# Kernel tuning notes

Measured on AMD Instinct MI355X. Metric: run time of the kernel, lower is better.

Reference implementation:

```python
import jax, jax.numpy as jnp
import numpy as np

HEAD_DIM = 128
NUM_Q_HEAD = 32
NUM_KV_HEAD = 8
GROUP_SIZE = 128
EPS = 1e-5
WINDOW = 512
CAP = 50.0
CLIP_L, CLIP_R = -0.01, 1.01
SCALE = 1.0 / np.sqrt(HEAD_DIM)
NEG = -1e9


def group_rmsnorm(x, gamma, gsz, eps):
    # x: [B, S, H]; per-group RMS over contiguous chunks of size gsz, then learned scale
    b, s, h = x.shape
    xg = x.reshape(b, s, h // gsz, gsz)
    rms = jnp.sqrt(jnp.mean(xg * xg, axis=-1, keepdims=True) + eps)
    return (xg / rms).reshape(b, s, h) * gamma


def setup_inputs() -> dict:
    key = jax.random.key(0)
    k1, k2, k3, k4, k5 = jax.random.split(key, 5)
    B, S = 2, 2048
    q = jax.random.normal(k1, (B, S, NUM_Q_HEAD, HEAD_DIM), dtype=jnp.float32)
    k = jax.random.normal(k2, (B, S, NUM_KV_HEAD, HEAD_DIM), dtype=jnp.float32)
    v = jax.random.normal(k3, (B, S, NUM_KV_HEAD, HEAD_DIM), dtype=jnp.float32)
    # GroupRMSNorm weights ~ U(init_range) = U(-1, 1)
    gamma_q = jax.random.uniform(k4, (NUM_Q_HEAD * HEAD_DIM,), dtype=jnp.float32, minval=-1.0, maxval=1.0)
    gamma_k = jax.random.uniform(k5, (NUM_KV_HEAD * HEAD_DIM,), dtype=jnp.float32, minval=-1.0, maxval=1.0)
    return {"q": q, "k": k, "v": v, "gamma_q": gamma_q, "gamma_k": gamma_k}


def reference(q, k, v, gamma_q, gamma_k):
    B, Sq, Hq, D = q.shape
    Sk, Hkv = k.shape[1], k.shape[2]
    # QK GroupRMSNorm on flattened hidden dim
    qn = group_rmsnorm(q.reshape(B, Sq, Hq * D), gamma_q, GROUP_SIZE, EPS).reshape(B, Sq, Hq, D)
    kn = group_rmsnorm(k.reshape(B, Sk, Hkv * D), gamma_k, GROUP_SIZE, EPS).reshape(B, Sk, Hkv, D)
    # GQA: repeat_interleave kv heads to match q heads
    rep = Hq // Hkv
    kr = jnp.repeat(kn, rep, axis=2)
    vr = jnp.repeat(v, rep, axis=2)
    # scores: [B, H, Sq, Sk]
    logits = jnp.einsum('bqhd,bkhd->bhqk', qn, kr) * SCALE
    # softmax capping (temperature path skipped when cap is set)
    logits = jnp.tanh(logits / CAP) * CAP
    # causal + sliding-window mask (aligned at sequence end)
    i = jnp.arange(Sq)[:, None]
    j = jnp.arange(Sk)[None, :]
    pos = i + (Sk - Sq)
    allowed = (j <= pos) & (pos - j <= WINDOW)
    logits = jnp.where(allowed, logits, NEG)
    probs = jax.nn.softmax(logits.astype(jnp.float32), axis=-1)
    # softmax clipping: clamp(probs * (r - l) + l, 0, 1)
    probs = jnp.clip(probs * (CLIP_R - CLIP_L) + CLIP_L, 0.0, 1.0)
    # output: [B, Sq, H, D]
    o = jnp.einsum('bhqk,bkhd->bqhd', probs.astype(q.dtype), vr)
    return o
```

## Files before the change

kernel.cpp:

```cpp
#include <hip/hip_runtime.h>

#define SEQ     2048
#define NQH     32
#define NKV     8
#define HD      128
#define WINDOW  512
#define QT      64
#define EPS_F   1e-5f
#define CQ2     0.12752981793f
#define PSTR    72

#define KN_OFF  0ull
#define VT_OFF  8388608ull

#define ROWPAT(r, hg) ((((r) & 3) + 8 * ((r) >> 2)) + 4 * (hg))

#define WAIT_BAR_4() asm volatile("s_waitcnt vmcnt(4)\n\ts_barrier" ::: "memory")
#define WAIT_BAR_0() asm volatile("s_waitcnt vmcnt(0)\n\ts_barrier" ::: "memory")
#define LGKM_BAR()  asm volatile("s_waitcnt lgkmcnt(0)\n\ts_barrier" ::: "memory")

using bf16x4 = __attribute__((ext_vector_type(4))) __bf16;
using bf16x8 = __attribute__((ext_vector_type(8))) __bf16;
using f32x16 = __attribute__((ext_vector_type(16))) float;

__device__ __forceinline__ void dma16(const void* g, void* l) {
    __builtin_amdgcn_global_load_lds(
        (const __attribute__((address_space(1))) unsigned int*)g,
        (__attribute__((address_space(3))) unsigned int*)l, 16, 0, 0);
}

__global__ __launch_bounds__(256)
void prep(const float* __restrict__ k, const float* __restrict__ v,
          const float* __restrict__ gk,
          __bf16* __restrict__ kn, __bf16* __restrict__ vt)
{
    const int blk = blockIdx.x;
    const int tid = threadIdx.x;
    if (blk < 512) {
        const int l16  = tid & 15;
        const int rsub = tid >> 4;
        #pragma unroll
        for (int it = 0; it < 4; it++) {
            const int row = blk * 64 + it * 16 + rsub;
            const float* src = k + (size_t)row * HD + l16 * 8;
            const float* g   = gk + (row & 7) * HD + l16 * 8;
            float4 a  = *(const float4*)(src);
            float4 b4 = *(const float4*)(src + 4);
            float ss = a.x*a.x + a.y*a.y + a.z*a.z + a.w*a.w
                     + b4.x*b4.x + b4.y*b4.y + b4.z*b4.z + b4.w*b4.w;
            ss += __shfl_xor(ss, 1); ss += __shfl_xor(ss, 2);
            ss += __shfl_xor(ss, 4); ss += __shfl_xor(ss, 8);
            const float rs = rsqrtf(ss * (1.f / 128.f) + EPS_F);
            float4 g0 = *(const float4*)(g);
            float4 g1 = *(const float4*)(g + 4);
            bf16x8 o;
            o[0] = (__bf16)(a.x  * rs * g0.x);  o[1] = (__bf16)(a.y  * rs * g0.y);
            o[2] = (__bf16)(a.z  * rs * g0.z);  o[3] = (__bf16)(a.w  * rs * g0.w);
            o[4] = (__bf16)(b4.x * rs * g1.x);  o[5] = (__bf16)(b4.y * rs * g1.y);
            o[6] = (__bf16)(b4.z * rs * g1.z);  o[7] = (__bf16)(b4.w * rs * g1.w);
            *(bf16x8*)(kn + (size_t)row * HD + l16 * 8) = o;
        }
    } else {
        const int blk2 = blk - 512;
        const int b    = blk2 >> 9;
        const int kvh  = (blk2 >> 6) & 7;
        const int sc   = (blk2 >> 2) & 15;
        const int dc   = blk2 & 3;
        const int s0   = sc * 128;
        const int d0   = dc * 32;
        const int c    = tid & 7;
        const int r    = tid >> 3;

        float xs[4][4];
        const float* src = v + ((size_t)(b * SEQ + s0 + r * 4) * NKV + kvh) * HD
                           + d0 + c * 4;
        #pragma unroll
        for (int i = 0; i < 4; i++) {
            float4 x = *(const float4*)(src + (size_t)i * (NKV * HD));
            xs[i][0] = x.x; xs[i][1] = x.y; xs[i][2] = x.z; xs[i][3] = x.w;
        }
        __bf16* dstb = vt + ((size_t)((b * NKV + kvh) * HD + d0 + c * 4)) * SEQ
                       + s0 + r * 4;
        #pragma unroll
        for (int u = 0; u < 4; u++) {
            bf16x4 o;
            o[0] = (__bf16)xs[0][u]; o[1] = (__bf16)xs[1][u];
            o[2] = (__bf16)xs[2][u]; o[3] = (__bf16)xs[3][u];
            *(bf16x4*)(dstb + (size_t)u * SEQ) = o;
        }
    }
}

__global__ __launch_bounds__(256, 2)
void swa_main(const float* __restrict__ q, const __bf16* __restrict__ kn,
              const __bf16* __restrict__ vt, const float* __restrict__ gq,
              float* __restrict__ out)
{
    __shared__ __align__(16) __bf16 sKV[3][QT * HD];
    __shared__ __align__(16) __bf16 sP[QT * PSTR];
    __shared__ float sLp[2][QT];
    __shared__ float sInvL[QT];

    const int wg   = blockIdx.x;
    const int qt   = wg & 31;
    const int h    = (wg >> 5) & 31;
    const int b    = wg >> 10;
    const int kvh  = h >> 2;
    const int i0   = qt * QT;
    const int tid  = threadIdx.x;
    const int lane = tid & 63;
    const int wave = tid >> 6;
    const int mhalf = wave & 1;
    const int nhalf = wave >> 1;
    const int m    = lane & 31;
    const int hg   = lane >> 5;

    const char* k_src[4];  const char* v_src[4];
    int kq_off[4];  int v_off[4];
    {
        const char* kn_head = (const char*)kn + ((size_t)b * SEQ * NKV + kvh) * 256;
        const char* vt_head = (const char*)vt + ((size_t)(b * NKV + kvh) * HD) * (SEQ * 2);
        #pragma unroll
        for (int i = 0; i < 4; i++) {
            const int chunk = wave * 4 + i;
            {
                const int r    = chunk * 4 + (lane >> 4);
                const int cpos = lane & 15;
                const int c    = (cpos & 8) | ((cpos ^ r) & 7);
                k_src[i]  = kn_head + (size_t)r * (NKV * HD * 2) + c * 16;
                kq_off[i] = chunk * 1024;
            }
            {
                const int r    = chunk * 8 + (lane >> 3);
                const int cpos = lane & 7;
                const int c    = cpos ^ (r & 7);
                v_src[i] = vt_head + (size_t)r * (SEQ * 2) + c * 16;
                v_off[i] = chunk * 1024;
            }
        }
    }

    const int t_lo   = (i0 >= WINDOW ? (i0 - WINDOW) : 0) >> 6;
    const int t_hi   = i0 >> 6;
    const int ttbias = t_hi - 8;
    const int krow   = nhalf * 32 + m;
    const size_t kstride = (size_t)64 * (NKV * HD * 2);

    {
        const size_t ko = (size_t)t_lo * kstride;
        char* dst0 = (char*)&sKV[t_lo % 3][0];
        #pragma unroll
        for (int i = 0; i < 4; i++) dma16(k_src[i] + ko, dst0 + kq_off[i]);
        if (t_lo < t_hi) {
            char* dst1 = (char*)&sKV[(t_lo + 1) % 3][0];
            #pragma unroll
            for (int i = 0; i < 4; i++) dma16(k_src[i] + ko + kstride, dst1 + kq_off[i]);
        }
    }

    bf16x8 qf[8];
    {
        const int qrow = i0 + mhalf * 32 + m;
        const float* qp = q + ((size_t)(b * SEQ + qrow) * NQH + h) * HD;
        float4 qb[16];
        float ss = 0.0f;
        #pragma unroll
        for (int kf = 0; kf < 8; kf++) {
            const int d0 = kf * 16 + hg * 8;
            float4 a  = *(const float4*)(qp + d0);
            float4 b4 = *(const float4*)(qp + d0 + 4);
            qb[kf * 2] = a; qb[kf * 2 + 1] = b4;
            ss += a.x*a.x + a.y*a.y + a.z*a.z + a.w*a.w
                + b4.x*b4.x + b4.y*b4.y + b4.z*b4.z + b4.w*b4.w;
        }
        ss += __shfl_xor(ss, 32);
        const float rs = rsqrtf(ss * (1.f / 128.f) + EPS_F) * CQ2;
        const float* gp = gq + h * HD;
        #pragma unroll
        for (int kf = 0; kf < 8; kf++) {
            const int d0 = kf * 16 + hg * 8;
            float4 g0 = *(const float4*)(gp + d0);
            float4 g1 = *(const float4*)(gp + d0 + 4);
            bf16x8 f;
            f[0] = (__bf16)(qb[kf*2].x   * rs * g0.x);
            f[1] = (__bf16)(qb[kf*2].y   * rs * g0.y);
            f[2] = (__bf16)(qb[kf*2].z   * rs * g0.z);
            f[3] = (__bf16)(qb[kf*2].w   * rs * g0.w);
            f[4] = (__bf16)(qb[kf*2+1].x * rs * g1.x);
            f[5] = (__bf16)(qb[kf*2+1].y * rs * g1.y);
            f[6] = (__bf16)(qb[kf*2+1].z * rs * g1.z);
            f[7] = (__bf16)(qb[kf*2+1].w * rs * g1.w);
            qf[kf] = f;
        }
    }

    float lacc[16];
    #pragma unroll
    for (int i = 0; i < 16; i++) lacc[i] = 0.f;
    bf16x8 ec[9][2];

    #pragma unroll
    for (int tt = 0; tt < 9; tt++) {
        const int t = ttbias + tt;
        if (t >= t_lo) {
            if (t < t_hi) { WAIT_BAR_4(); } else { WAIT_BAR_0(); }
            const __bf16* kb = &sKV[t % 3][0];
            bf16x8 bk[8];
            #pragma unroll
            for (int kf = 0; kf < 8; kf++) {
                const int cc  = kf * 2 + hg;
                const int pos = (cc & 8) | ((cc ^ krow) & 7);
                bk[kf] = *(const bf16x8*)(kb + krow * HD + pos * 8);
            }
            if (t + 2 <= t_hi) {
                const size_t ko = (size_t)(t + 2) * kstride;
                char* dstp = (char*)&sKV[(t + 2) % 3][0];
                #pragma unroll
                for (int i = 0; i < 4; i++) dma16(k_src[i] + ko, dstp + kq_off[i]);
            }
            f32x16 c;
            #pragma unroll
            for (int i = 0; i < 16; i++) c[i] = 0.f;
            #pragma unroll
            for (int kf = 0; kf < 8; kf++)
                c = __builtin_amdgcn_mfma_f32_32x32x16_bf16(qf[kf], bk[kf], c, 0, 0, 0);

            const bool do_mask = (t == t_hi) || (t == t_lo && i0 >= WINDOW);
            const int kj = t * 64 + krow;
            float e[16];
            #pragma unroll
            for (int r = 0; r < 16; r++) {
                float ev = __builtin_amdgcn_exp2f(c[r]);
                if (do_mask) {
                    const int qi = i0 + mhalf * 32 + ROWPAT(r, hg);
                    ev = ((unsigned)(qi - kj) <= WINDOW) ? ev : 0.f;
                }
                lacc[r] += ev;
                e[r] = ev;
            }
            bf16x8 p0v, p1v;
            #pragma unroll
            for (int j = 0; j < 8; j++) { p0v[j] = (__bf16)e[j]; p1v[j] = (__bf16)e[8 + j]; }
            ec[tt][0] = p0v;  ec[tt][1] = p1v;
        }
    }

    #pragma unroll
    for (int r = 0; r < 16; r++) {
        float l = lacc[r];
        l += __shfl_xor(l, 1);  l += __shfl_xor(l, 2);  l += __shfl_xor(l, 4);
        l += __shfl_xor(l, 8);  l += __shfl_xor(l, 16);
        lacc[r] = l;
    }
    if (m == 0) {
        #pragma unroll
        for (int r = 0; r < 16; r++)
            sLp[nhalf][mhalf * 32 + ROWPAT(r, hg)] = lacc[r];
    }
    LGKM_BAR();
    {
        const size_t vo = (size_t)t_lo * 128;
        char* dst0 = (char*)&sKV[t_lo % 3][0];
        #pragma unroll
        for (int i = 0; i < 4; i++) dma16(v_src[i] + vo, dst0 + v_off[i]);
        if (t_lo < t_hi) {
            char* dst1 = (char*)&sKV[(t_lo + 1) % 3][0];
            #pragma unroll
            for (int i = 0; i < 4; i++) dma16(v_src[i] + vo + 128, dst1 + v_off[i]);
        }
    }
    if (tid < QT) sInvL[tid] = __builtin_amdgcn_rcpf(sLp[0][tid] + sLp[1][tid]);
    LGKM_BAR();

    float ar[16];
    #pragma unroll
    for (int r = 0; r < 16; r++) ar[r] = 1.02f * sInvL[mhalf * 32 + ROWPAT(r, hg)];

    f32x16 o0, o1;
    #pragma unroll
    for (int i = 0; i < 16; i++) { o0[i] = 0.f; o1[i] = 0.f; }

    #pragma unroll
    for (int tt = 0; tt < 9; tt++) {
        const int t = ttbias + tt;
        if (t >= t_lo) {
            if (t < t_hi) { WAIT_BAR_4(); } else { WAIT_BAR_0(); }
            #pragma unroll
            for (int half = 0; half < 2; half++) {
                #pragma unroll
                for (int j = 0; j < 8; j++) {
                    const int r = half * 8 + j;
                    const float ee = (float)ec[tt][half][j];
                    const float f = fminf(fmaxf(fmaf(ee, ar[r], -0.01f), 0.f), 1.f);
                    sP[(mhalf * 32 + ROWPAT(r, hg)) * PSTR + krow] = (__bf16)f;
                }
            }
            LGKM_BAR();
            const __bf16* vb = &sKV[t % 3][0];
            bf16x8 pa[4], vf0[4], vf1[4];
            #pragma unroll
            for (int kf = 0; kf < 4; kf++) {
                pa[kf] = *(const bf16x8*)&sP[(mhalf * 32 + m) * PSTR + kf * 16 + hg * 8];
                const int cc = kf * 2 + hg;
                const int row0 = nhalf * 64 + m;
                const int row1 = nhalf * 64 + 32 + m;
                vf0[kf] = *(const bf16x8*)(vb + row0 * 64 + ((cc ^ row0) & 7) * 8);
                vf1[kf] = *(const bf16x8*)(vb + row1 * 64 + ((cc ^ row1) & 7) * 8);
            }
            if (t + 2 <= t_hi) {
                const size_t vo = (size_t)(t + 2) * 128;
                char* dstp = (char*)&sKV[(t + 2) % 3][0];
                #pragma unroll
                for (int i = 0; i < 4; i++) dma16(v_src[i] + vo, dstp + v_off[i]);
            }
            #pragma unroll
            for (int kf = 0; kf < 4; kf++) {
                o0 = __builtin_amdgcn_mfma_f32_32x32x16_bf16(pa[kf], vf0[kf], o0, 0, 0, 0);
                o1 = __builtin_amdgcn_mfma_f32_32x32x16_bf16(pa[kf], vf1[kf], o1, 0, 0, 0);
            }
        }
    }

    #pragma unroll
    for (int r = 0; r < 16; r++) {
        const int row = i0 + mhalf * 32 + ROWPAT(r, hg);
        float* op = out + ((size_t)(b * SEQ + row) * NQH + h) * HD + nhalf * 64 + m;
        op[0]  = o0[r];
        op[32] = o1[r];
    }
}

extern "C" void kernel_launch(void* const* d_in, const int* in_sizes, int n_in,
                              void* d_out, int out_size, void* d_ws, size_t ws_size,
                              hipStream_t stream) {
    const float* q  = (const float*)d_in[0];
    const float* k  = (const float*)d_in[1];
    const float* v  = (const float*)d_in[2];
    const float* gq = (const float*)d_in[3];
    const float* gk = (const float*)d_in[4];
    float* out = (float*)d_out;

    __bf16* kn = (__bf16*)((char*)d_ws + KN_OFF);
    __bf16* vt = (__bf16*)((char*)d_ws + VT_OFF);

    prep<<<1536, 256, 0, stream>>>(k, v, gk, kn, vt);
    swa_main<<<2 * NQH * (SEQ / QT), 256, 0, stream>>>(q, kn, vt, gq, out);
}
```

Baseline: 214.2 us.

## Restructure attention kernel: 128-row Q tiles, per-wave rows, recompute QK, register P

```diff
diff --git a/kernel.cpp b/kernel.cpp
--- a/kernel.cpp
+++ b/kernel.cpp
@@ -8,14 +8,12 @@
 #define QT      64
 #define EPS_F   1e-5f
 #define CQ2     0.12752981793f
-#define PSTR    72
 
 #define KN_OFF  0ull
 #define VT_OFF  8388608ull
 
 #define ROWPAT(r, hg) ((((r) & 3) + 8 * ((r) >> 2)) + 4 * (hg))
 
-#define WAIT_BAR_4() asm volatile("s_waitcnt vmcnt(4)\n\ts_barrier" ::: "memory")
 #define WAIT_BAR_0() asm volatile("s_waitcnt vmcnt(0)\n\ts_barrier" ::: "memory")
 #define LGKM_BAR()  asm volatile("s_waitcnt lgkmcnt(0)\n\ts_barrier" ::: "memory")
 
@@ -27,6 +25,15 @@
     __builtin_amdgcn_global_load_lds(
         (const __attribute__((address_space(1))) unsigned int*)g,
         (__attribute__((address_space(3))) unsigned int*)l, 16, 0, 0);
+}
+
+__device__ __forceinline__ unsigned cvtpk(float lo, float hi) {
+    unsigned r;
+    asm("v_cvt_pk_bf16_f32 %0, %1, %2" : "=v"(r) : "v"(lo), "v"(hi));
+    return r;
+}
+__device__ __forceinline__ void pl32swap(unsigned &a, unsigned &b) {
+    asm("v_permlane32_swap_b32 %0, %1" : "+v"(a), "+v"(b));
 }
 
 __global__ __launch_bounds__(256)
@@ -70,7 +77,6 @@
         const int d0   = dc * 32;
         const int c    = tid & 7;
         const int r    = tid >> 3;
-
         float xs[4][4];
         const float* src = v + ((size_t)(b * SEQ + s0 + r * 4) * NKV + kvh) * HD
                            + d0 + c * 4;
@@ -96,24 +102,29 @@
               const __bf16* __restrict__ vt, const float* __restrict__ gq,
               float* __restrict__ out)
 {
-    __shared__ __align__(16) __bf16 sKV[3][QT * HD];
-    __shared__ __align__(16) __bf16 sP[QT * PSTR];
-    __shared__ float sLp[2][QT];
-    __shared__ float sInvL[QT];
-
-    const int wg   = blockIdx.x;
-    const int qt   = wg & 31;
-    const int h    = (wg >> 5) & 31;
-    const int b    = wg >> 10;
-    const int kvh  = h >> 2;
-    const int i0   = qt * QT;
+    __shared__ __align__(16) __bf16 sK0[QT * HD];
+    __shared__ __align__(16) __bf16 sK1[QT * HD];
+    __shared__ __align__(16) __bf16 sV0[QT * HD];
+    __shared__ __align__(16) __bf16 sV1[QT * HD];
+
+    const int wg0  = blockIdx.x;
+    const int xcd  = wg0 & 7;
+    const int gi   = wg0 >> 3;
+    const int pair = xcd * 2 + (gi >> 6);
+    const int rr_  = gi & 63;
+    const int qt   = rr_ & 15;
+    const int hsub = rr_ >> 4;
+    const int b    = pair >> 3;
+    const int kvh  = pair & 7;
+    const int h    = kvh * 4 + hsub;
+    const int i0   = qt * 128;
+
     const int tid  = threadIdx.x;
     const int lane = tid & 63;
     const int wave = tid >> 6;
-    const int mhalf = wave & 1;
-    const int nhalf = wave >> 1;
     const int m    = lane & 31;
     const int hg   = lane >> 5;
+    const int sb   = i0 + wave * 32;
 
     const char* k_src[4];  const char* v_src[4];
     int kq_off[4];  int v_off[4];
@@ -140,27 +151,22 @@
         }
     }
 
-    const int t_lo   = (i0 >= WINDOW ? (i0 - WINDOW) : 0) >> 6;
-    const int t_hi   = i0 >> 6;
-    const int ttbias = t_hi - 8;
-    const int krow   = nhalf * 32 + m;
+    const int t_lo  = (i0 >= WINDOW) ? (i0 - WINDOW) >> 6 : 0;
+    const int t_hi  = (i0 >> 6) + 1;
+    const int tw_lo = (sb >= WINDOW) ? (sb - WINDOW) >> 6 : 0;
+    const int tw_hi = sb >> 6;
     const size_t kstride = (size_t)64 * (NKV * HD * 2);
 
     {
         const size_t ko = (size_t)t_lo * kstride;
-        char* dst0 = (char*)&sKV[t_lo % 3][0];
-        #pragma unroll
-        for (int i = 0; i < 4; i++) dma16(k_src[i] + ko, dst0 + kq_off[i]);
-        if (t_lo < t_hi) {
-            char* dst1 = (char*)&sKV[(t_lo + 1) % 3][0];
-            #pragma unroll
-            for (int i = 0; i < 4; i++) dma16(k_src[i] + ko + kstride, dst1 + kq_off[i]);
-        }
+        char* dst = (char*)((t_lo & 1) ? sK1 : sK0);
+        #pragma unroll
+        for (int i = 0; i < 4; i++) dma16(k_src[i] + ko, dst + kq_off[i]);
     }
 
     bf16x8 qf[8];
     {
-        const int qrow = i0 + mhalf * 32 + m;
+        const int qrow = sb + m;
         const float* qp = q + ((size_t)(b * SEQ + qrow) * NQH + h) * HD;
         float4 qb[16];
         float ss = 0.0f;
@@ -194,139 +200,167 @@
         }
     }
 
-    float lacc[16];
+    float Lp = 0.f;
+    for (int t = t_lo; t <= t_hi; ++t) {
+        WAIT_BAR_0();
+        const __bf16* kb = (t & 1) ? sK1 : sK0;
+        bf16x8 bka[8], bkb[8];
+        #pragma unroll
+        for (int kf = 0; kf < 8; kf++) {
+            const int cc  = kf * 2 + hg;
+            const int pos = (cc & 8) | ((cc ^ m) & 7);
+            bka[kf] = *(const bf16x8*)(kb + m * HD + pos * 8);
+            bkb[kf] = *(const bf16x8*)(kb + (32 + m) * HD + pos * 8);
+        }
+        if (t < t_hi) {
+            const size_t ko = (size_t)(t + 1) * kstride;
+            char* dst = (char*)(((t + 1) & 1) ? sK1 : sK0);
+            #pragma unroll
+            for (int i = 0; i < 4; i++) dma16(k_src[i] + ko, dst + kq_off[i]);
+        }
+        if (t >= tw_lo && t <= tw_hi) {
+            f32x16 c0, c1;
+            #pragma unroll
+            for (int i = 0; i < 16; i++) { c0[i] = 0.f; c1[i] = 0.f; }
+            __builtin_amdgcn_s_setprio(1);
+            #pragma unroll
+            for (int kf = 0; kf < 8; kf++) {
+                c0 = __builtin_amdgcn_mfma_f32_32x32x16_bf16(bka[kf], qf[kf], c0, 0, 0, 0);
+                c1 = __builtin_amdgcn_mfma_f32_32x32x16_bf16(bkb[kf], qf[kf], c1, 0, 0, 0);
+            }
+            __builtin_amdgcn_s_setprio(0);
+            const bool dm = !((t * 64 + 63 <= sb) && (sb + 31 - t * 64 <= WINDOW));
+            const int qi = sb + m;
+            #pragma unroll
+            for (int r = 0; r < 16; r++) {
+                float e0 = __builtin_amdgcn_exp2f(c0[r]);
+                float e1 = __builtin_amdgcn_exp2f(c1[r]);
+                if (dm) {
+                    const int kj = t * 64 + ROWPAT(r, hg);
+                    e0 = ((unsigned)(qi - kj) <= WINDOW) ? e0 : 0.f;
+                    e1 = ((unsigned)(qi - (kj + 32)) <= WINDOW) ? e1 : 0.f;
+                }
+                Lp += e0 + e1;
+            }
+        }
+    }
+    Lp += __shfl_xor(Lp, 32);
+    const float arq = 1.02f * __builtin_amdgcn_rcpf(Lp);
+
+    LGKM_BAR();
+
+    {
+        const size_t ko = (size_t)t_lo * kstride;
+        const size_t vo = (size_t)t_lo * 128;
+        char* kd = (char*)((t_lo & 1) ? sK1 : sK0);
+        char* vd = (char*)((t_lo & 1) ? sV1 : sV0);
+        #pragma unroll
+        for (int i = 0; i < 4; i++) dma16(k_src[i] + ko, kd + kq_off[i]);
+        #pragma unroll
+        for (int i = 0; i < 4; i++) dma16(v_src[i] + vo, vd + v_off[i]);
+    }
+
+    f32x16 oa[4];
     #pragma unroll
-    for (int i = 0; i < 16; i++) lacc[i] = 0.f;
-    bf16x8 ec[9][2];
-
-    #pragma unroll
-    for (int tt = 0; tt < 9; tt++) {
-        const int t = ttbias + tt;
-        if (t >= t_lo) {
-            if (t < t_hi) { WAIT_BAR_4(); } else { WAIT_BAR_0(); }
-            const __bf16* kb = &sKV[t % 3][0];
-            bf16x8 bk[8];
+    for (int dc = 0; dc < 4; dc++)
+        #pragma unroll
+        for (int i = 0; i < 16; i++) oa[dc][i] = 0.f;
+
+    for (int t = t_lo; t <= t_hi; ++t) {
+        WAIT_BAR_0();
+        const __bf16* kb = (t & 1) ? sK1 : sK0;
+        const __bf16* vb = (t & 1) ? sV1 : sV0;
+        bf16x8 bka[8], bkb[8];
+        #pragma unroll
+        for (int kf = 0; kf < 8; kf++) {
+            const int cc  = kf * 2 + hg;
+            const int pos = (cc & 8) | ((cc ^ m) & 7);
+            bka[kf] = *(const bf16x8*)(kb + m * HD + pos * 8);
+            bkb[kf] = *(const bf16x8*)(kb + (32 + m) * HD + pos * 8);
+        }
+        if (t < t_hi) {
+            const size_t ko = (size_t)(t + 1) * kstride;
+            const size_t vo = (size_t)(t + 1) * 128;
+            char* kd = (char*)(((t + 1) & 1) ? sK1 : sK0);
+            char* vd = (char*)(((t + 1) & 1) ? sV1 : sV0);
+            #pragma unroll
+            for (int i = 0; i < 4; i++) dma16(k_src[i] + ko, kd + kq_off[i]);
+            #pragma unroll
+            for (int i = 0; i < 4; i++) dma16(v_src[i] + vo, vd + v_off[i]);
+        }
+        if (t >= tw_lo && t <= tw_hi) {
+            f32x16 c0, c1;
+            #pragma unroll
+            for (int i = 0; i < 16; i++) { c0[i] = 0.f; c1[i] = 0.f; }
+            __builtin_amdgcn_s_setprio(1);
             #pragma unroll
             for (int kf = 0; kf < 8; kf++) {
-                const int cc  = kf * 2 + hg;
-                const int pos = (cc & 8) | ((cc ^ krow) & 7);
-                bk[kf] = *(const bf16x8*)(kb + krow * HD + pos * 8);
-            }
-            if (t + 2 <= t_hi) {
-                const size_t ko = (size_t)(t + 2) * kstride;
-                char* dstp = (char*)&sKV[(t + 2) % 3][0];
+                c0 = __builtin_amdgcn_mfma_f32_32x32x16_bf16(bka[kf], qf[kf], c0, 0, 0, 0);
+                c1 = __builtin_amdgcn_mfma_f32_32x32x16_bf16(bkb[kf], qf[kf], c1, 0, 0, 0);
+            }
+            __builtin_amdgcn_s_setprio(0);
+            const bool dm = !((t * 64 + 63 <= sb) && (sb + 31 - t * 64 <= WINDOW));
+            const int qi = sb + m;
+            float f0[16], f1[16];
+            #pragma unroll
+            for (int r = 0; r < 16; r++) {
+                float e0 = __builtin_amdgcn_exp2f(c0[r]);
+                float e1 = __builtin_amdgcn_exp2f(c1[r]);
+                if (dm) {
+                    const int kj = t * 64 + ROWPAT(r, hg);
+                    e0 = ((unsigned)(qi - kj) <= WINDOW) ? e0 : 0.f;
+                    e1 = ((unsigned)(qi - (kj + 32)) <= WINDOW) ? e1 : 0.f;
+                }
+                f0[r] = fminf(fmaxf(fmaf(e0, arq, -0.01f), 0.f), 1.f);
+                f1[r] = fminf(fmaxf(fmaf(e1, arq, -0.01f), 0.f), 1.f);
+            }
+            bf16x8 pa[4];
+            #pragma unroll
+            for (int kk = 0; kk < 4; kk++) {
+                const int base = (kk & 1) * 8;
+                unsigned A0, A1, B0, B1;
+                if (kk < 2) {
+                    A0 = cvtpk(f0[base + 0], f0[base + 1]);
+                    A1 = cvtpk(f0[base + 2], f0[base + 3]);
+                    B0 = cvtpk(f0[base + 4], f0[base + 5]);
+                    B1 = cvtpk(f0[base + 6], f0[base + 7]);
+                } else {
+                    A0 = cvtpk(f1[base + 0], f1[base + 1]);
+                    A1 = cvtpk(f1[base + 2], f1[base + 3]);
+                    B0 = cvtpk(f1[base + 4], f1[base + 5]);
+                    B1 = cvtpk(f1[base + 6], f1[base + 7]);
+                }
+                pl32swap(A0, B0);
+                pl32swap(A1, B1);
+                union { int4 i4; bf16x8 v; } u;
+                u.i4.x = (int)A0; u.i4.y = (int)A1; u.i4.z = (int)B0; u.i4.w = (int)B1;
+                pa[kk] = u.v;
+            }
+            __builtin_amdgcn_s_setprio(1);
+            #pragma unroll
+            for (int dc = 0; dc < 4; dc++) {
+                const int d = dc * 32 + m;
+                bf16x8 vf[4];
                 #pragma unroll
-                for (int i = 0; i < 4; i++) dma16(k_src[i] + ko, dstp + kq_off[i]);
-            }
-            f32x16 c;
-            #pragma unroll
-            for (int i = 0; i < 16; i++) c[i] = 0.f;
-            #pragma unroll
-            for (int kf = 0; kf < 8; kf++)
-                c = __builtin_amdgcn_mfma_f32_32x32x16_bf16(qf[kf], bk[kf], c, 0, 0, 0);
-
-            const bool do_mask = (t == t_hi) || (t == t_lo && i0 >= WINDOW);
-            const int kj = t * 64 + krow;
-            float e[16];
-            #pragma unroll
-            for (int r = 0; r < 16; r++) {
-                float ev = __builtin_amdgcn_exp2f(c[r]);
-                if (do_mask) {
-                    const int qi = i0 + mhalf * 32 + ROWPAT(r, hg);
-                    ev = ((unsigned)(qi - kj) <= WINDOW) ? ev : 0.f;
+                for (int kf = 0; kf < 4; kf++) {
+                    const int slot = ((kf * 2 + hg) ^ d) & 7;
+                    vf[kf] = *(const bf16x8*)(vb + d * 64 + slot * 8);
                 }
-                lacc[r] += ev;
-                e[r] = ev;
-            }
-            bf16x8 p0v, p1v;
-            #pragma unroll
-            for (int j = 0; j < 8; j++) { p0v[j] = (__bf16)e[j]; p1v[j] = (__bf16)e[8 + j]; }
-            ec[tt][0] = p0v;  ec[tt][1] = p1v;
-        }
-    }
-
+                #pragma unroll
+                for (int kf = 0; kf < 4; kf++)
+                    oa[dc] = __builtin_amdgcn_mfma_f32_32x32x16_bf16(pa[kf], vf[kf], oa[dc], 0, 0, 0);
+            }
+            __builtin_amdgcn_s_setprio(0);
+        }
+    }
+
+    float* ob = out + ((size_t)(b * SEQ + sb) * NQH + h) * HD + m;
     #pragma unroll
     for (int r = 0; r < 16; r++) {
-        float l = lacc[r];
-        l += __shfl_xor(l, 1);  l += __shfl_xor(l, 2);  l += __shfl_xor(l, 4);
-        l += __shfl_xor(l, 8);  l += __shfl_xor(l, 16);
-        lacc[r] = l;
-    }
-    if (m == 0) {
-        #pragma unroll
-        for (int r = 0; r < 16; r++)
-            sLp[nhalf][mhalf * 32 + ROWPAT(r, hg)] = lacc[r];
-    }
-    LGKM_BAR();
-    {
-        const size_t vo = (size_t)t_lo * 128;
-        char* dst0 = (char*)&sKV[t_lo % 3][0];
-        #pragma unroll
-        for (int i = 0; i < 4; i++) dma16(v_src[i] + vo, dst0 + v_off[i]);
-        if (t_lo < t_hi) {
-            char* dst1 = (char*)&sKV[(t_lo + 1) % 3][0];
-            #pragma unroll
-            for (int i = 0; i < 4; i++) dma16(v_src[i] + vo + 128, dst1 + v_off[i]);
-        }
-    }
-    if (tid < QT) sInvL[tid] = __builtin_amdgcn_rcpf(sLp[0][tid] + sLp[1][tid]);
-    LGKM_BAR();
-
-    float ar[16];
-    #pragma unroll
-    for (int r = 0; r < 16; r++) ar[r] = 1.02f * sInvL[mhalf * 32 + ROWPAT(r, hg)];
-
-    f32x16 o0, o1;
-    #pragma unroll
-    for (int i = 0; i < 16; i++) { o0[i] = 0.f; o1[i] = 0.f; }
-
-    #pragma unroll
-    for (int tt = 0; tt < 9; tt++) {
-        const int t = ttbias + tt;
-        if (t >= t_lo) {
-            if (t < t_hi) { WAIT_BAR_4(); } else { WAIT_BAR_0(); }
-            #pragma unroll
-            for (int half = 0; half < 2; half++) {
-                #pragma unroll
-                for (int j = 0; j < 8; j++) {
-                    const int r = half * 8 + j;
-                    const float ee = (float)ec[tt][half][j];
-                    const float f = fminf(fmaxf(fmaf(ee, ar[r], -0.01f), 0.f), 1.f);
-                    sP[(mhalf * 32 + ROWPAT(r, hg)) * PSTR + krow] = (__bf16)f;
-                }
-            }
-            LGKM_BAR();
-            const __bf16* vb = &sKV[t % 3][0];
-            bf16x8 pa[4], vf0[4], vf1[4];
-            #pragma unroll
-            for (int kf = 0; kf < 4; kf++) {
-                pa[kf] = *(const bf16x8*)&sP[(mhalf * 32 + m) * PSTR + kf * 16 + hg * 8];
-                const int cc = kf * 2 + hg;
-                const int row0 = nhalf * 64 + m;
-                const int row1 = nhalf * 64 + 32 + m;
-                vf0[kf] = *(const bf16x8*)(vb + row0 * 64 + ((cc ^ row0) & 7) * 8);
-                vf1[kf] = *(const bf16x8*)(vb + row1 * 64 + ((cc ^ row1) & 7) * 8);
-            }
-            if (t + 2 <= t_hi) {
-                const size_t vo = (size_t)(t + 2) * 128;
-                char* dstp = (char*)&sKV[(t + 2) % 3][0];
-                #pragma unroll
-                for (int i = 0; i < 4; i++) dma16(v_src[i] + vo, dstp + v_off[i]);
-            }
-            #pragma unroll
-            for (int kf = 0; kf < 4; kf++) {
-                o0 = __builtin_amdgcn_mfma_f32_32x32x16_bf16(pa[kf], vf0[kf], o0, 0, 0, 0);
-                o1 = __builtin_amdgcn_mfma_f32_32x32x16_bf16(pa[kf], vf1[kf], o1, 0, 0, 0);
-            }
-        }
-    }
-
-    #pragma unroll
-    for (int r = 0; r < 16; r++) {
-        const int row = i0 + mhalf * 32 + ROWPAT(r, hg);
-        float* op = out + ((size_t)(b * SEQ + row) * NQH + h) * HD + nhalf * 64 + m;
-        op[0]  = o0[r];
-        op[32] = o1[r];
+        const int rowoff = ROWPAT(r, hg) * (NQH * HD);
+        #pragma unroll
+        for (int dc = 0; dc < 4; dc++)
+            ob[rowoff + dc * 32] = oa[dc][r];
     }
 }
 
@@ -344,5 +378,5 @@
     __bf16* vt = (__bf16*)((char*)d_ws + VT_OFF);
 
     prep<<<1536, 256, 0, stream>>>(k, v, gk, kn, vt);
-    swa_main<<<2 * NQH * (SEQ / QT), 256, 0, stream>>>(q, kn, vt, gq, out);
-}
+    swa_main<<<1024, 256, 0, stream>>>(q, kn, vt, gq, out);
+}
```

After: 218.8 us. 2.1% more time.
